# Kernel optimization log

Hardware: AMD Instinct MI355X
Metric: run time of the kernel (lower is better)

Reference implementation:

```python
import jax, jax.numpy as jnp
import numpy as np

DIM = 2048
HQ = 32
HKV = 8
HD = DIM // HQ  # 64
B, T = 2, 2048


def _rope_tables(key_unused):
    # Standard RoPE tables: cos/sin of shape [B, T, HD]
    inv_freq = 1.0 / (10000.0 ** (np.arange(0, HD, 2, dtype=np.float32) / HD))
    t = np.arange(T, dtype=np.float32)
    freqs = np.outer(t, inv_freq)                 # [T, HD/2]
    emb = np.concatenate([freqs, freqs], axis=-1)  # [T, HD]
    cos = jnp.asarray(np.cos(emb))[None].repeat(B, axis=0)
    sin = jnp.asarray(np.sin(emb))[None].repeat(B, axis=0)
    return cos, sin


def setup_inputs() -> dict:
    key = jax.random.key(0)
    ks = jax.random.split(key, 8)
    s_in = 1.0 / np.sqrt(DIM)
    x = jax.random.normal(ks[0], (B, T, DIM), dtype=jnp.float32)
    cos, sin = _rope_tables(None)
    # Linear weights stored as [in, out] (transposed vs torch)
    Wq = jax.random.normal(ks[1], (DIM, HQ * HD), dtype=jnp.float32) * s_in
    bq = jnp.zeros((HQ * HD,), dtype=jnp.float32)
    Wk = jax.random.normal(ks[2], (DIM, HKV * HD), dtype=jnp.float32) * s_in
    bk = jnp.zeros((HKV * HD,), dtype=jnp.float32)
    Wv = jax.random.normal(ks[3], (DIM, HKV * HD), dtype=jnp.float32) * s_in
    bv = jnp.zeros((HKV * HD,), dtype=jnp.float32)
    Wo = jax.random.normal(ks[4], (HQ * HD, DIM), dtype=jnp.float32) * s_in
    return {"x": x, "cos": cos, "sin": sin, "Wq": Wq, "bq": bq,
            "Wk": Wk, "bk": bk, "Wv": Wv, "bv": bv, "Wo": Wo}


def _rotate_half(u):
    u1, u2 = jnp.split(u, 2, axis=-1)
    return jnp.concatenate([-u2, u1], axis=-1)


def reference(x, cos, sin, Wq, bq, Wk, bk, Wv, bv, Wo):
    Bx, Tx, D = x.shape
    g = HQ // HKV  # group size (queries per kv head)
    q = (x @ Wq + bq).reshape(Bx, Tx, HQ, HD).transpose(0, 2, 1, 3)   # [B,Hq,T,d]
    k = (x @ Wk + bk).reshape(Bx, Tx, HKV, HD).transpose(0, 2, 1, 3)  # [B,Hkv,T,d]
    v = (x @ Wv + bv).reshape(Bx, Tx, HKV, HD).transpose(0, 2, 1, 3)
    c = cos[:, None, :, :]  # [B,1,T,d]
    s = sin[:, None, :, :]
    q = q * c + _rotate_half(q) * s
    k = k * c + _rotate_half(k) * s
    # GQA: group query heads over shared KV heads instead of repeat_interleave
    qg = q.reshape(Bx, HKV, g, Tx, HD)
    scale = 1.0 / np.sqrt(HD)
    scores = jnp.einsum('bkgtd,bksd->bkgts', qg, k) * scale  # [B,Hkv,g,T,T]
    causal = jnp.tril(jnp.ones((Tx, Tx), dtype=bool))
    scores = jnp.where(causal, scores, jnp.finfo(scores.dtype).min)
    probs = jax.nn.softmax(scores, axis=-1)
    out = jnp.einsum('bkgts,bksd->bkgtd', probs, v)           # [B,Hkv,g,T,d]
    out = out.reshape(Bx, HQ, Tx, HD).transpose(0, 2, 1, 3).reshape(Bx, Tx, HQ * HD)
    return out @ Wo
```

## Files before the change

### kernel.cpp

```cpp
#include <hip/hip_runtime.h>


typedef short s8v __attribute__((ext_vector_type(8)));
typedef float f4v __attribute__((ext_vector_type(4)));

__device__ __forceinline__ unsigned short f2bf(float f) {
  unsigned int u = __float_as_uint(f);
  u += 0x7fffu + ((u >> 16) & 1u);
  return (unsigned short)(u >> 16);
}

__device__ __forceinline__ unsigned int pk_bf16(float a, float b) {
#if __has_builtin(__builtin_amdgcn_cvt_pk_bf16_f32)
  auto r = __builtin_amdgcn_cvt_pk_bf16_f32(a, b);
  return *(unsigned int*)&r;
#else
  return (unsigned int)f2bf(a) | ((unsigned int)f2bf(b) << 16);
#endif
}

__device__ __forceinline__ void llds16(const void* g, void* l) {
  __builtin_amdgcn_global_load_lds(
      (__attribute__((address_space(1))) void*)(g),
      (__attribute__((address_space(3))) void*)(l), 16, 0, 0);
}

__global__ __launch_bounds__(256) void prep_k(const float* __restrict__ x,
    const float* __restrict__ Wq, const float* __restrict__ Wk,
    const float* __restrict__ Wv, const float* __restrict__ Wo,
    unsigned short* __restrict__ xb, unsigned short* __restrict__ Wt,
    unsigned short* __restrict__ Wot) {
  const int tid = threadIdx.x;
  int bid = blockIdx.x;
  if (bid < 8192) {
    const int i = bid * 256 + tid;
    float4 v = ((const float4*)x)[i];
    ushort4 o;
    o.x = f2bf(v.x); o.y = f2bf(v.y); o.z = f2bf(v.z); o.w = f2bf(v.w);
    ((ushort4*)xb)[i] = o;
    return;
  }
  bid -= 8192;
  const float* src; unsigned short* dst; int srcW, bx, by;
  if (bid < 4096)      { src = Wq; dst = Wt;                        srcW = 2048; bx = bid & 63;        by = bid >> 6; }
  else if (bid < 5120) { src = Wk; dst = Wt + (size_t)2048 * 2048;  srcW = 512;  bx = (bid - 4096) & 15; by = (bid - 4096) >> 4; }
  else if (bid < 6144) { src = Wv; dst = Wt + (size_t)2560 * 2048;  srcW = 512;  bx = (bid - 5120) & 15; by = (bid - 5120) >> 4; }
  else                 { src = Wo; dst = Wot;                       srcW = 2048; bx = (bid - 6144) & 63; by = (bid - 6144) >> 6; }
  __shared__ float tile[32][33];
  const int tx = tid & 31, ty = tid >> 5;
  const int xg = bx * 32 + tx;
  const int ybase = by * 32;
#pragma unroll
  for (int j = 0; j < 32; j += 8)
    tile[ty + j][tx] = src[(size_t)(ybase + ty + j) * srcW + xg];
  __syncthreads();
  const int x2 = ybase + tx;
  const int y2 = bx * 32 + ty;
#pragma unroll
  for (int j = 0; j < 32; j += 8)
    dst[(size_t)(y2 + j) * 2048 + x2] = f2bf(tile[tx][ty + j]);
}

__device__ __forceinline__ void gemm128(const unsigned short* __restrict__ A,
                                        const unsigned short* __restrict__ Bt,
                                        int K, int m0, int n0,
                                        unsigned short* As, unsigned short* Bs,
                                        f4v acc[4][4]) {
  const int tid = threadIdx.x;
  const int lane = tid & 63;
  const int w = tid >> 6;
  const int wm = w >> 1, wn = w & 1;
  const int c = lane & 15, quad = lane >> 4;
  const int srow = tid >> 2;
  const int scol = ((tid & 3) ^ ((tid >> 3) & 3)) * 8;
  const int ca = (quad ^ ((c >> 1) & 3)) * 8;
  for (int k0 = 0; k0 < K; k0 += 32) {
    const unsigned short* ga = A + (size_t)(m0 + srow) * K + k0 + scol;
    const unsigned short* gb = Bt + (size_t)(n0 + srow) * K + k0 + scol;
    llds16(ga,          As + w * 512);
    llds16(ga + 64 * K, As + 2048 + w * 512);
    llds16(gb,          Bs + w * 512);
    llds16(gb + 64 * K, Bs + 2048 + w * 512);
    __syncthreads();
    s8v a[4], b[4];
#pragma unroll
    for (int i = 0; i < 4; ++i)
      a[i] = *(const s8v*)&As[(wm * 64 + i * 16 + c) * 32 + ca];
#pragma unroll
    for (int i = 0; i < 4; ++i)
      b[i] = *(const s8v*)&Bs[(wn * 64 + i * 16 + c) * 32 + ca];
#pragma unroll
    for (int mb = 0; mb < 4; ++mb)
#pragma unroll
      for (int nb = 0; nb < 4; ++nb)
        acc[mb][nb] = __builtin_amdgcn_mfma_f32_16x16x32_bf16(a[mb], b[nb], acc[mb][nb], 0, 0, 0);
    __syncthreads();
  }
}

__global__ __launch_bounds__(256) void gemm_qkv(const unsigned short* __restrict__ A,
    const unsigned short* __restrict__ Bt,
    const float* __restrict__ bq, const float* __restrict__ bk, const float* __restrict__ bv,
    const float* __restrict__ cosp, const float* __restrict__ sinp,
    unsigned short* __restrict__ Qb, unsigned short* __restrict__ Kb,
    unsigned short* __restrict__ Vt) {
  __shared__ unsigned short As[4096], Bs[4096];
  const f4v fzero = {0.f, 0.f, 0.f, 0.f};
  f4v acc[4][4];
#pragma unroll
  for (int i = 0; i < 4; ++i)
#pragma unroll
    for (int j = 0; j < 4; ++j) acc[i][j] = fzero;
  const int m0 = blockIdx.y * 128, n0 = blockIdx.x * 128;
  gemm128(A, Bt, 2048, m0, n0, As, Bs, acc);

  const int tid = threadIdx.x, lane = tid & 63, w = tid >> 6;
  const int wm = w >> 1, wn = w & 1, c = lane & 15, quad = lane >> 4;
  const int nbase = n0 + wn * 64;
  const float QSC = 0.125f * 1.44269504089f;
#pragma unroll
  for (int mb = 0; mb < 4; ++mb) {
#pragma unroll
    for (int r = 0; r < 4; ++r) {
      const int row = m0 + wm * 64 + mb * 16 + quad * 4 + r;
      const int b = row >> 11, t = row & 2047;
      if (nbase < 2048) {
        const int h = nbase >> 6;
        const size_t ob = ((size_t)(b * 32 + h) * 2048 + t) * 64;
        const float* cb = cosp + (size_t)row * 64;
        const float* sb = sinp + (size_t)row * 64;
#pragma unroll
        for (int nb = 0; nb < 2; ++nb) {
          const int d0 = nb * 16 + c, d1 = d0 + 32;
          const float v0 = acc[mb][nb][r] + bq[nbase + d0];
          const float v1 = acc[mb][nb + 2][r] + bq[nbase + d1];
          Qb[ob + d0] = f2bf((v0 * cb[d0] - v1 * sb[d0]) * QSC);
          Qb[ob + d1] = f2bf((v1 * cb[d1] + v0 * sb[d1]) * QSC);
        }
      } else if (nbase < 2560) {
        const int h = (nbase - 2048) >> 6;
        const size_t ob = ((size_t)(b * 8 + h) * 2048 + t) * 64;
        const float* cb = cosp + (size_t)row * 64;
        const float* sb = sinp + (size_t)row * 64;
#pragma unroll
        for (int nb = 0; nb < 2; ++nb) {
          const int d0 = nb * 16 + c, d1 = d0 + 32;
          const float v0 = acc[mb][nb][r] + bk[nbase - 2048 + d0];
          const float v1 = acc[mb][nb + 2][r] + bk[nbase - 2048 + d1];
          Kb[ob + d0] = f2bf(v0 * cb[d0] - v1 * sb[d0]);
          Kb[ob + d1] = f2bf(v1 * cb[d1] + v0 * sb[d1]);
        }
      } else {
        const int h = (nbase - 2560) >> 6;
        const size_t vb = (size_t)(b * 8 + h) * 64;
        const int tl = t & 63;
        const int tp = (t & ~63) | (((tl & 15) << 2) | (tl >> 4));
#pragma unroll
        for (int nb = 0; nb < 4; ++nb) {
          const int d = nb * 16 + c;
          Vt[(vb + d) * 2048 + tp] = f2bf(acc[mb][nb][r] + bv[nbase - 2560 + d]);
        }
      }
    }
  }
}

__global__ __launch_bounds__(256) void attn_k(const unsigned short* __restrict__ Qb,
                                              const unsigned short* __restrict__ Kb,
                                              const unsigned short* __restrict__ Vt,
                                              unsigned short* __restrict__ An) {
  __shared__ unsigned short QPs[4096];
  __shared__ unsigned short Ks[2][4096], Vs[2][4096];
  const int tid = threadIdx.x, lane = tid & 63, w = tid >> 6;
  const int c = lane & 15, quad = lane >> 4;
  const int bh = blockIdx.y;
  const int b = bh >> 5, h = bh & 31, kvh = h >> 2;
  const int qt = gridDim.x - 1 - blockIdx.x;
  const int q0 = qt * 64;
  const unsigned short* gQ = Qb + ((size_t)bh * 2048 + q0) * 64;
  const unsigned short* gK = Kb + (size_t)(b * 8 + kvh) * 2048 * 64;
  const unsigned short* gV = Vt + (size_t)(b * 8 + kvh) * 64 * 2048;

  const int r0 = tid >> 3;
  const int ch8 = ((tid & 7) ^ (r0 & 7)) * 8;

  llds16(gQ + r0 * 64 + ch8,        QPs + w * 512);
  llds16(gQ + (r0 + 32) * 64 + ch8, QPs + 2048 + w * 512);
  llds16(gK + r0 * 64 + ch8,        Ks[0] + w * 512);
  llds16(gK + (r0 + 32) * 64 + ch8, Ks[0] + 2048 + w * 512);
  llds16(gV + (size_t)r0 * 2048 + ch8,        Vs[0] + w * 512);
  llds16(gV + (size_t)(r0 + 32) * 2048 + ch8, Vs[0] + 2048 + w * 512);
  __syncthreads();

  const int xq0 = (quad ^ (c & 7)) * 8;
  const int xq1 = ((quad + 4) ^ (c & 7)) * 8;
  const s8v aq0 = *(const s8v*)&QPs[(w * 16 + c) * 64 + xq0];
  const s8v aq1 = *(const s8v*)&QPs[(w * 16 + c) * 64 + xq1];

  const f4v fzero = {0.f, 0.f, 0.f, 0.f};
  f4v O[4];
  float lrp[4];
#pragma unroll
  for (int i = 0; i < 4; ++i) { O[i] = fzero; lrp[i] = 0.f; }

  const int ntiles = qt + 1;
  for (int it = 0; it < ntiles; ++it) {
    const int cur = it & 1;
    if (it + 1 < ntiles) {
      const int s1 = (it + 1) * 64, nxt = cur ^ 1;
      llds16(gK + (size_t)(s1 + r0) * 64 + ch8,      Ks[nxt] + w * 512);
      llds16(gK + (size_t)(s1 + r0 + 32) * 64 + ch8, Ks[nxt] + 2048 + w * 512);
      llds16(gV + (size_t)r0 * 2048 + s1 + ch8,        Vs[nxt] + w * 512);
      llds16(gV + (size_t)(r0 + 32) * 2048 + s1 + ch8, Vs[nxt] + 2048 + w * 512);
    }

    f4v S[4];
#pragma unroll
    for (int nb = 0; nb < 4; ++nb) {
      const s8v bk0 = *(const s8v*)&Ks[cur][(nb * 16 + c) * 64 + xq0];
      const s8v bk1 = *(const s8v*)&Ks[cur][(nb * 16 + c) * 64 + xq1];
      f4v z = fzero;
      z = __builtin_amdgcn_mfma_f32_16x16x32_bf16(aq0, bk0, z, 0, 0, 0);
      z = __builtin_amdgcn_mfma_f32_16x16x32_bf16(aq1, bk1, z, 0, 0, 0);
      S[nb] = z;
    }

    const bool diag = (it == qt);
#pragma unroll
    for (int r = 0; r < 4; ++r) {
      const int rloc = quad * 4 + r;
      float p[4];
#pragma unroll
      for (int nb = 0; nb < 4; ++nb) {
        float sv = S[nb][r];
        if (diag && (nb * 16 + c > w * 16 + rloc)) sv = -1e30f;
        p[nb] = __builtin_amdgcn_exp2f(sv);
      }
      lrp[r] += (p[0] + p[1]) + (p[2] + p[3]);
      uint2 pk2;
      pk2.x = pk_bf16(p[0], p[1]);
      pk2.y = pk_bf16(p[2], p[3]);
      *(uint2*)&QPs[w * 1024 + rloc * 64 + (((c >> 1) ^ (rloc & 7)) * 8) + (c & 1) * 4] = pk2;
    }
    asm volatile("s_waitcnt lgkmcnt(0)" ::: "memory");

    const s8v ap0 = *(const s8v*)&QPs[w * 1024 + c * 64 + xq0];
    const s8v ap1 = *(const s8v*)&QPs[w * 1024 + c * 64 + xq1];
#pragma unroll
    for (int nbd = 0; nbd < 4; ++nbd) {
      const s8v bv0 = *(const s8v*)&Vs[cur][(nbd * 16 + c) * 64 + xq0];
      const s8v bv1 = *(const s8v*)&Vs[cur][(nbd * 16 + c) * 64 + xq1];
      O[nbd] = __builtin_amdgcn_mfma_f32_16x16x32_bf16(ap0, bv0, O[nbd], 0, 0, 0);
      O[nbd] = __builtin_amdgcn_mfma_f32_16x16x32_bf16(ap1, bv1, O[nbd], 0, 0, 0);
    }
    __syncthreads();
  }

#pragma unroll
  for (int r = 0; r < 4; ++r) {
    float ps = lrp[r];
    ps += __shfl_xor(ps, 1, 64);
    ps += __shfl_xor(ps, 2, 64);
    ps += __shfl_xor(ps, 4, 64);
    ps += __shfl_xor(ps, 8, 64);
    const float inv = 1.0f / ps;
    const int t = q0 + w * 16 + quad * 4 + r;
    const size_t rowb = ((size_t)b * 2048 + t) * 2048 + h * 64;
#pragma unroll
    for (int nbd = 0; nbd < 4; ++nbd)
      An[rowb + nbd * 16 + c] = f2bf(O[nbd][r] * inv);
  }
}

__global__ __launch_bounds__(256) void gemm_out(const unsigned short* __restrict__ A,
                                                const unsigned short* __restrict__ Bt,
                                                float* __restrict__ C) {
  __shared__ unsigned short As[4096], Bs[4096];
  const f4v fzero = {0.f, 0.f, 0.f, 0.f};
  f4v acc[4][4];
#pragma unroll
  for (int i = 0; i < 4; ++i)
#pragma unroll
    for (int j = 0; j < 4; ++j) acc[i][j] = fzero;
  const int m0 = blockIdx.y * 128, n0 = blockIdx.x * 128;
  gemm128(A, Bt, 2048, m0, n0, As, Bs, acc);
  const int tid = threadIdx.x, lane = tid & 63, w = tid >> 6;
  const int wm = w >> 1, wn = w & 1, c = lane & 15, quad = lane >> 4;
#pragma unroll
  for (int mb = 0; mb < 4; ++mb)
#pragma unroll
    for (int r = 0; r < 4; ++r) {
      const int row = m0 + wm * 64 + mb * 16 + quad * 4 + r;
#pragma unroll
      for (int nb = 0; nb < 4; ++nb)
        C[(size_t)row * 2048 + n0 + wn * 64 + nb * 16 + c] = acc[mb][nb][r];
    }
}

extern "C" void kernel_launch(void* const* d_in, const int* in_sizes, int n_in,
                              void* d_out, int out_size, void* d_ws, size_t ws_size,
                              hipStream_t stream) {
  const float* x    = (const float*)d_in[0];
  const float* cosp = (const float*)d_in[1];
  const float* sinp = (const float*)d_in[2];
  const float* Wq   = (const float*)d_in[3];
  const float* bq   = (const float*)d_in[4];
  const float* Wk   = (const float*)d_in[5];
  const float* bk   = (const float*)d_in[6];
  const float* Wv   = (const float*)d_in[7];
  const float* bv   = (const float*)d_in[8];
  const float* Wo   = (const float*)d_in[9];
  float* out = (float*)d_out;

  char* ws = (char*)d_ws;
  unsigned short* xb  = (unsigned short*)(ws);
  unsigned short* Wt  = (unsigned short*)(ws + 16777216);
  unsigned short* Wot = (unsigned short*)(ws + 29360128);
  unsigned short* Qb  = (unsigned short*)(ws + 37748736);
  unsigned short* Kb  = (unsigned short*)(ws + 54525952);
  unsigned short* Vt  = (unsigned short*)(ws + 58720256);
  unsigned short* An  = (unsigned short*)(ws + 62914560);

  prep_k<<<18432, 256, 0, stream>>>(x, Wq, Wk, Wv, Wo, xb, Wt, Wot);
  gemm_qkv<<<dim3(24, 32), 256, 0, stream>>>(xb, Wt, bq, bk, bv, cosp, sinp, Qb, Kb, Vt);
  attn_k<<<dim3(32, 64), 256, 0, stream>>>(Qb, Kb, Vt, An);
  gemm_out<<<dim3(16, 32), 256, 0, stream>>>(An, Wot, out);
}
```

Measured before the change: 379.2 us.

## Double-buffer LDS tiles in the QKV and output GEMMs to overlap loads with MFMA

The shared 128x128 GEMM helper now uses two LDS buffers per operand. While MFMAs run on the current k-slice, the next k-slice is fetched with global_load_lds into the other buffer, which removes one of the two barriers' worth of load latency from each iteration. LDS use per block doubles to 32KB, which may lower occupancy. The remaining end-of-iteration sync also has to cover the asynchronous prefetch for the pipeline to be correct.

```diff
diff --git a/kernel.cpp b/kernel.cpp
--- a/kernel.cpp
+++ b/kernel.cpp
@@ -61,11 +61,12 @@
     dst[(size_t)(y2 + j) * 2048 + x2] = f2bf(tile[tx][ty + j]);
 }
 
-__device__ __forceinline__ void gemm128(const unsigned short* __restrict__ A,
-                                        const unsigned short* __restrict__ Bt,
-                                        int K, int m0, int n0,
-                                        unsigned short* As, unsigned short* Bs,
-                                        f4v acc[4][4]) {
+__device__ __forceinline__ void gemm128_db(const unsigned short* __restrict__ A,
+                                           const unsigned short* __restrict__ Bt,
+                                           int K, int m0, int n0,
+                                           unsigned short (*As)[4096],
+                                           unsigned short (*Bs)[4096],
+                                           f4v acc[4][4]) {
   const int tid = threadIdx.x;
   const int lane = tid & 63;
   const int w = tid >> 6;
@@ -74,21 +75,32 @@
   const int srow = tid >> 2;
   const int scol = ((tid & 3) ^ ((tid >> 3) & 3)) * 8;
   const int ca = (quad ^ ((c >> 1) & 3)) * 8;
-  for (int k0 = 0; k0 < K; k0 += 32) {
-    const unsigned short* ga = A + (size_t)(m0 + srow) * K + k0 + scol;
-    const unsigned short* gb = Bt + (size_t)(n0 + srow) * K + k0 + scol;
-    llds16(ga,          As + w * 512);
-    llds16(ga + 64 * K, As + 2048 + w * 512);
-    llds16(gb,          Bs + w * 512);
-    llds16(gb + 64 * K, Bs + 2048 + w * 512);
-    __syncthreads();
+  const unsigned short* ga0 = A + (size_t)(m0 + srow) * K + scol;
+  const unsigned short* gb0 = Bt + (size_t)(n0 + srow) * K + scol;
+
+  llds16(ga0,          As[0] + w * 512);
+  llds16(ga0 + 64 * K, As[0] + 2048 + w * 512);
+  llds16(gb0,          Bs[0] + w * 512);
+  llds16(gb0 + 64 * K, Bs[0] + 2048 + w * 512);
+  __syncthreads();
+
+  const int niter = K >> 5;
+  for (int it = 0; it < niter; ++it) {
+    const int cur = it & 1;
+    if (it + 1 < niter) {
+      const int kk = (it + 1) << 5, nxt = cur ^ 1;
+      llds16(ga0 + kk,          As[nxt] + w * 512);
+      llds16(ga0 + kk + 64 * K, As[nxt] + 2048 + w * 512);
+      llds16(gb0 + kk,          Bs[nxt] + w * 512);
+      llds16(gb0 + kk + 64 * K, Bs[nxt] + 2048 + w * 512);
+    }
     s8v a[4], b[4];
 #pragma unroll
     for (int i = 0; i < 4; ++i)
-      a[i] = *(const s8v*)&As[(wm * 64 + i * 16 + c) * 32 + ca];
+      a[i] = *(const s8v*)&As[cur][(wm * 64 + i * 16 + c) * 32 + ca];
 #pragma unroll
     for (int i = 0; i < 4; ++i)
-      b[i] = *(const s8v*)&Bs[(wn * 64 + i * 16 + c) * 32 + ca];
+      b[i] = *(const s8v*)&Bs[cur][(wn * 64 + i * 16 + c) * 32 + ca];
 #pragma unroll
     for (int mb = 0; mb < 4; ++mb)
 #pragma unroll
@@ -104,7 +116,7 @@
     const float* __restrict__ cosp, const float* __restrict__ sinp,
     unsigned short* __restrict__ Qb, unsigned short* __restrict__ Kb,
     unsigned short* __restrict__ Vt) {
-  __shared__ unsigned short As[4096], Bs[4096];
+  __shared__ unsigned short As[2][4096], Bs[2][4096];
   const f4v fzero = {0.f, 0.f, 0.f, 0.f};
   f4v acc[4][4];
 #pragma unroll
@@ -112,7 +124,7 @@
 #pragma unroll
     for (int j = 0; j < 4; ++j) acc[i][j] = fzero;
   const int m0 = blockIdx.y * 128, n0 = blockIdx.x * 128;
-  gemm128(A, Bt, 2048, m0, n0, As, Bs, acc);
+  gemm128_db(A, Bt, 2048, m0, n0, As, Bs, acc);
 
   const int tid = threadIdx.x, lane = tid & 63, w = tid >> 6;
   const int wm = w >> 1, wn = w & 1, c = lane & 15, quad = lane >> 4;
@@ -275,7 +287,7 @@
 __global__ __launch_bounds__(256) void gemm_out(const unsigned short* __restrict__ A,
                                                 const unsigned short* __restrict__ Bt,
                                                 float* __restrict__ C) {
-  __shared__ unsigned short As[4096], Bs[4096];
+  __shared__ unsigned short As[2][4096], Bs[2][4096];
   const f4v fzero = {0.f, 0.f, 0.f, 0.f};
   f4v acc[4][4];
 #pragma unroll
@@ -283,7 +295,7 @@
 #pragma unroll
     for (int j = 0; j < 4; ++j) acc[i][j] = fzero;
   const int m0 = blockIdx.y * 128, n0 = blockIdx.x * 128;
-  gemm128(A, Bt, 2048, m0, n0, As, Bs, acc);
+  gemm128_db(A, Bt, 2048, m0, n0, As, Bs, acc);
   const int tid = threadIdx.x, lane = tid & 63, w = tid >> 6;
   const int wm = w >> 1, wn = w & 1, c = lane & 15, quad = lane >> 4;
 #pragma unroll
```

Measured after the change: 365.7 us. 1.04x faster.
